# Performance work log

Measured on AMD Instinct MI355X. Metric: run time of the kernel, lower is better.

## Reference

```python
import jax, jax.numpy as jnp
import numpy as np

KSIZE = 8
STRIDE = 4
HEADS = 8
DIM_HEAD = 32
EPS = 1e-5


def _layernorm(x, g, b):
    m = jnp.mean(x, axis=-1, keepdims=True)
    v = jnp.mean(jnp.square(x - m), axis=-1, keepdims=True)
    return (x - m) / jnp.sqrt(v + EPS) * g + b


def setup_inputs() -> dict:
    key = jax.random.key(0)
    ks = jax.random.split(key, 4)
    B, H, W, C = 8, 64, 64, 256
    inner = HEADS * DIM_HEAD  # 256
    x = jax.random.normal(ks[0], (B, H, W, C), dtype=jnp.float32)
    return {
        "x": x,
        "ln1_g": jnp.ones((C,), jnp.float32),
        "ln1_b": jnp.zeros((C,), jnp.float32),
        "ln2_g": jnp.ones((C,), jnp.float32),
        "ln2_b": jnp.zeros((C,), jnp.float32),
        "w_qkv": jax.random.normal(ks[1], (C, inner * 3), jnp.float32) * 0.02,
        "w_out": jax.random.normal(ks[2], (inner, C), jnp.float32) * 0.02,
        "b_out": jnp.zeros((C,), jnp.float32),
    }


def reference(x, ln1_g, ln1_b, ln2_g, ln2_b, w_qkv, w_out, b_out):
    B, H, W, C = x.shape
    k, s = KSIZE, STRIDE
    nH = (H - k) // s + 1
    nW = (W - k) // s + 1
    L = nH * nW
    n = k * k  # tokens per window

    # window index grids (im2col / unfold)
    rows = jnp.arange(nH)[:, None] * s + jnp.arange(k)[None, :]  # [nH, k]
    cols = jnp.arange(nW)[:, None] * s + jnp.arange(k)[None, :]  # [nW, k]
    ridx = rows[:, None, :, None]  # [nH,1,k,1]
    cidx = cols[None, :, None, :]  # [1,nW,1,k]

    # unfold: [B, nH, nW, k, k, C] -> [(B L), (k k), C]
    patches = x[:, ridx, cidx, :].reshape(B * L, n, C)

    # LocalAttention2D.norm then AttentionBlock.norm
    p = _layernorm(patches, ln1_g, ln1_b)
    h = _layernorm(p, ln2_g, ln2_b)

    qkv = h @ w_qkv  # [(B L), n, 3*inner]
    q, kk, v = jnp.split(qkv, 3, axis=-1)
    q = q.reshape(B * L, n, HEADS, DIM_HEAD)
    kk = kk.reshape(B * L, n, HEADS, DIM_HEAD)
    v = v.reshape(B * L, n, HEADS, DIM_HEAD)

    scale = DIM_HEAD ** -0.5
    dots = jnp.einsum('bnhd,bmhd->bhnm', q, kk) * scale
    attn = jax.nn.softmax(dots, axis=-1)
    o = jnp.einsum('bhnm,bmhd->bnhd', attn, v).reshape(B * L, n, HEADS * DIM_HEAD)
    o = o @ w_out + b_out  # [(B L), n, C]

    # fold (col2im overlap-add)
    o = o.reshape(B, nH, nW, k, k, C)
    out = jnp.zeros((B, H, W, C), x.dtype).at[:, ridx, cidx, :].add(o)

    # normalization: fold(unfold(ones)) == overlap counts
    counts = jnp.zeros((H, W), x.dtype).at[ridx, cidx].add(1.0)
    return out / counts[None, :, :, None]
```

## Files before the change

kernel.cpp:

```cpp
#include <hip/hip_runtime.h>
#include <hip/hip_bf16.h>
#include <cstdint>
#include <cstddef>

#define LN_EPS 1e-5f
#define B_    8
#define HW_   64
#define C_    256
#define NTOK  (B_ * HW_ * HW_)
#define HEADS_ 8
#define DH_    32
#define NPATCH 15

__global__ __launch_bounds__(256) void ln_h_kernel(
    const float* __restrict__ x, const float* __restrict__ g1,
    const float* __restrict__ b1, const float* __restrict__ g2,
    const float* __restrict__ b2, float* __restrict__ h)
{
    const int gid  = blockIdx.x * 256 + threadIdx.x;
    const int tok  = gid >> 6;
    const int lane = gid & 63;
    if (tok >= NTOK) return;
    const float4 xv = reinterpret_cast<const float4*>(x + (size_t)tok * C_)[lane];
    float s  = xv.x + xv.y + xv.z + xv.w;
    float sq = xv.x*xv.x + xv.y*xv.y + xv.z*xv.z + xv.w*xv.w;
    for (int off = 32; off; off >>= 1) {
        s  += __shfl_xor(s, off);
        sq += __shfl_xor(sq, off);
    }
    const float m1 = s * (1.0f / 256.0f);
    const float r1 = rsqrtf(fmaxf(sq * (1.0f / 256.0f) - m1 * m1, 0.0f) + LN_EPS);
    const float4 g = reinterpret_cast<const float4*>(g1)[lane];
    const float4 b = reinterpret_cast<const float4*>(b1)[lane];
    const float y0 = (xv.x - m1) * r1 * g.x + b.x;
    const float y1 = (xv.y - m1) * r1 * g.y + b.y;
    const float y2 = (xv.z - m1) * r1 * g.z + b.z;
    const float y3 = (xv.w - m1) * r1 * g.w + b.w;
    float s2  = y0 + y1 + y2 + y3;
    float sq2 = y0*y0 + y1*y1 + y2*y2 + y3*y3;
    for (int off = 32; off; off >>= 1) {
        s2  += __shfl_xor(s2, off);
        sq2 += __shfl_xor(sq2, off);
    }
    const float m2 = s2 * (1.0f / 256.0f);
    const float r2 = rsqrtf(fmaxf(sq2 * (1.0f / 256.0f) - m2 * m2, 0.0f) + LN_EPS);
    const float4 G = reinterpret_cast<const float4*>(g2)[lane];
    const float4 B = reinterpret_cast<const float4*>(b2)[lane];
    float4 hv;
    hv.x = (y0 - m2) * r2 * G.x + B.x;
    hv.y = (y1 - m2) * r2 * G.y + B.y;
    hv.z = (y2 - m2) * r2 * G.z + B.z;
    hv.w = (y3 - m2) * r2 * G.w + B.w;
    reinterpret_cast<float4*>(h + (size_t)tok * C_)[lane] = hv;
}

__global__ __launch_bounds__(256) void qkv_h8_kernel(
    const float* __restrict__ h, const float* __restrict__ w, float* __restrict__ qkv)
{
    __shared__ float At[16][132];
    __shared__ float Bt[16][132];
    const int tid  = threadIdx.x;
    const int tok0 = blockIdx.y * 128;
    const int n0   = blockIdx.x * 128;
    const int ty = tid >> 4, tx = tid & 15;
    const int ar = tid >> 2, aseg = tid & 3;
    const int bk = tid >> 5, bn = tid & 31;
    const float* hrow0 = h + (size_t)(tok0 + ar) * C_;
    const float* hrow1 = h + (size_t)(tok0 + ar + 64) * C_;
    float acc[8][8] = {};
    for (int kk = 0; kk < 16; ++kk) {
        const int k0 = kk * 16;
        const float4 a0v = *reinterpret_cast<const float4*>(hrow0 + k0 + aseg * 4);
        const float4 a1v = *reinterpret_cast<const float4*>(hrow1 + k0 + aseg * 4);
        const float4 b0v = *reinterpret_cast<const float4*>(w + (size_t)(k0 + bk) * 768 + n0 + bn * 4);
        const float4 b1v = *reinterpret_cast<const float4*>(w + (size_t)(k0 + bk + 8) * 768 + n0 + bn * 4);
        __syncthreads();
        At[aseg*4+0][ar]    = a0v.x;
        At[aseg*4+1][ar]    = a0v.y;
        At[aseg*4+2][ar]    = a0v.z;
        At[aseg*4+3][ar]    = a0v.w;
        At[aseg*4+0][ar+64] = a1v.x;
        At[aseg*4+1][ar+64] = a1v.y;
        At[aseg*4+2][ar+64] = a1v.z;
        At[aseg*4+3][ar+64] = a1v.w;
        *reinterpret_cast<float4*>(&Bt[bk][bn*4])     = b0v;
        *reinterpret_cast<float4*>(&Bt[bk+8][bn*4])   = b1v;
        __syncthreads();
        #pragma unroll
        for (int k = 0; k < 16; ++k) {
            const float4 x0 = *reinterpret_cast<const float4*>(&At[k][ty*8]);
            const float4 x1 = *reinterpret_cast<const float4*>(&At[k][ty*8 + 4]);
            const float4 y0 = *reinterpret_cast<const float4*>(&Bt[k][tx*4]);
            const float4 y1 = *reinterpret_cast<const float4*>(&Bt[k][64 + tx*4]);
            const float a[8] = {x0.x, x0.y, x0.z, x0.w, x1.x, x1.y, x1.z, x1.w};
            const float b[8] = {y0.x, y0.y, y0.z, y0.w, y1.x, y1.y, y1.z, y1.w};
            #pragma unroll
            for (int i = 0; i < 8; ++i) {
                #pragma unroll
                for (int j = 0; j < 8; ++j)
                    acc[i][j] = fmaf(a[i], b[j], acc[i][j]);
            }
        }
    }
    #pragma unroll
    for (int i = 0; i < 8; ++i) {
        float* orow = qkv + (size_t)(tok0 + ty*8 + i) * 768 + n0;
        *reinterpret_cast<float4*>(orow + tx*4) =
            make_float4(acc[i][0], acc[i][1], acc[i][2], acc[i][3]);
        *reinterpret_cast<float4*>(orow + 64 + tx*4) =
            make_float4(acc[i][4], acc[i][5], acc[i][6], acc[i][7]);
    }
}

__global__ __launch_bounds__(256) void ln_stats_kernel(
    const float* __restrict__ x, const float* __restrict__ g1,
    const float* __restrict__ b1, float4* __restrict__ stats)
{
    const int gid  = blockIdx.x * 256 + threadIdx.x;
    const int tok  = gid >> 6;
    const int lane = gid & 63;
    if (tok >= NTOK) return;
    const float4 xv = reinterpret_cast<const float4*>(x + (size_t)tok * C_)[lane];
    float s  = xv.x + xv.y + xv.z + xv.w;
    float sq = xv.x*xv.x + xv.y*xv.y + xv.z*xv.z + xv.w*xv.w;
    for (int off = 32; off; off >>= 1) {
        s  += __shfl_xor(s, off);
        sq += __shfl_xor(sq, off);
    }
    const float m1 = s * (1.0f / 256.0f);
    const float r1 = rsqrtf(fmaxf(sq * (1.0f / 256.0f) - m1 * m1, 0.0f) + LN_EPS);
    const float4 g = reinterpret_cast<const float4*>(g1)[lane];
    const float4 b = reinterpret_cast<const float4*>(b1)[lane];
    const float y0 = (xv.x - m1) * r1 * g.x + b.x;
    const float y1 = (xv.y - m1) * r1 * g.y + b.y;
    const float y2 = (xv.z - m1) * r1 * g.z + b.z;
    const float y3 = (xv.w - m1) * r1 * g.w + b.w;
    float s2  = y0 + y1 + y2 + y3;
    float sq2 = y0*y0 + y1*y1 + y2*y2 + y3*y3;
    for (int off = 32; off; off >>= 1) {
        s2  += __shfl_xor(s2, off);
        sq2 += __shfl_xor(sq2, off);
    }
    const float m2 = s2 * (1.0f / 256.0f);
    const float r2 = rsqrtf(fmaxf(sq2 * (1.0f / 256.0f) - m2 * m2, 0.0f) + LN_EPS);
    if (lane == 0) stats[tok] = make_float4(m1, r1, m2, r2);
}

__global__ __launch_bounds__(256) void qkv_kernel(
    const float* __restrict__ x, const float4* __restrict__ stats,
    const float* __restrict__ g1, const float* __restrict__ b1,
    const float* __restrict__ g2, const float* __restrict__ b2,
    const float* __restrict__ w, float* __restrict__ qkv)
{
    __shared__ float At[16][72];
    __shared__ float Bt[16][64];
    const int tid  = threadIdx.x;
    const int tok0 = blockIdx.y * 64;
    const int n0   = blockIdx.x * 64;
    const int ty = tid >> 4, tx = tid & 15;
    const int st = tid >> 2, sseg = tid & 3;
    const int bk = tid >> 4, bx = tid & 15;
    const float4 s4 = stats[tok0 + st];
    const float* xrow = x + (size_t)(tok0 + st) * C_;
    float acc[4][4] = {};
    for (int kk = 0; kk < 16; ++kk) {
        const int k0 = kk * 16;
        const int ka = k0 + sseg * 4;
        const float4 xv  = *reinterpret_cast<const float4*>(xrow + ka);
        const float4 g1v = *reinterpret_cast<const float4*>(g1 + ka);
        const float4 b1v = *reinterpret_cast<const float4*>(b1 + ka);
        const float4 g2v = *reinterpret_cast<const float4*>(g2 + ka);
        const float4 b2v = *reinterpret_cast<const float4*>(b2 + ka);
        const float h0 = ((xv.x - s4.x)*s4.y*g1v.x + b1v.x - s4.z)*s4.w*g2v.x + b2v.x;
        const float h1 = ((xv.y - s4.x)*s4.y*g1v.y + b1v.y - s4.z)*s4.w*g2v.y + b2v.y;
        const float h2 = ((xv.z - s4.x)*s4.y*g1v.z + b1v.z - s4.z)*s4.w*g2v.z + b2v.z;
        const float h3 = ((xv.w - s4.x)*s4.y*g1v.w + b1v.w - s4.z)*s4.w*g2v.w + b2v.w;
        const float4 wv = *reinterpret_cast<const float4*>(w + (size_t)(k0 + bk) * 768 + n0 + bx * 4);
        __syncthreads();
        At[sseg*4+0][st] = h0;
        At[sseg*4+1][st] = h1;
        At[sseg*4+2][st] = h2;
        At[sseg*4+3][st] = h3;
        *reinterpret_cast<float4*>(&Bt[bk][bx*4]) = wv;
        __syncthreads();
        #pragma unroll
        for (int k = 0; k < 16; ++k) {
            const float4 a = *reinterpret_cast<const float4*>(&At[k][ty*4]);
            const float4 b = *reinterpret_cast<const float4*>(&Bt[k][tx*4]);
            acc[0][0] += a.x*b.x; acc[0][1] += a.x*b.y; acc[0][2] += a.x*b.z; acc[0][3] += a.x*b.w;
            acc[1][0] += a.y*b.x; acc[1][1] += a.y*b.y; acc[1][2] += a.y*b.z; acc[1][3] += a.y*b.w;
            acc[2][0] += a.z*b.x; acc[2][1] += a.z*b.y; acc[2][2] += a.z*b.z; acc[2][3] += a.z*b.w;
            acc[3][0] += a.w*b.x; acc[3][1] += a.w*b.y; acc[3][2] += a.w*b.z; acc[3][3] += a.w*b.w;
        }
    }
    #pragma unroll
    for (int r = 0; r < 4; ++r) {
        const float4 o = make_float4(acc[r][0], acc[r][1], acc[r][2], acc[r][3]);
        *reinterpret_cast<float4*>(qkv + (size_t)(tok0 + ty*4 + r) * 768 + n0 + tx*4) = o;
    }
}

__global__ __launch_bounds__(256) void attn_o_kernel(
    const float* __restrict__ qkv, float* __restrict__ obuf)
{
    __shared__ float smem[6784];
    float (*q_lds)[36] = reinterpret_cast<float(*)[36]>(smem);
    float (*kT)[68]    = reinterpret_cast<float(*)[68]>(smem + 2304);
    float (*v_lds)[36] = reinterpret_cast<float(*)[36]>(smem + 4480);
    float (*p_lds)[67] = reinterpret_cast<float(*)[67]>(smem);
    const int tid = threadIdx.x;
    const int b  = blockIdx.y;
    const int hd = blockIdx.z;
    const int pi = blockIdx.x / NPATCH;
    const int pj = blockIdx.x % NPATCH;
    const int t = tid >> 2, seg = tid & 3;
    const int pr = t >> 3, pc = t & 7;
    const size_t pixbase = ((size_t)((b * 64 + 4*pi + pr) * 64) + (4*pj + pc));
    {
        const size_t base = pixbase * 768 + hd * 32 + seg * 8;
        const float4 qa = *reinterpret_cast<const float4*>(qkv + base);
        const float4 qb = *reinterpret_cast<const float4*>(qkv + base + 4);
        const float4 ka = *reinterpret_cast<const float4*>(qkv + base + 256);
        const float4 kb = *reinterpret_cast<const float4*>(qkv + base + 260);
        const float4 va = *reinterpret_cast<const float4*>(qkv + base + 512);
        const float4 vb = *reinterpret_cast<const float4*>(qkv + base + 516);
        *reinterpret_cast<float4*>(&q_lds[t][seg*8    ]) = qa;
        *reinterpret_cast<float4*>(&q_lds[t][seg*8 + 4]) = qb;
        *reinterpret_cast<float4*>(&v_lds[t][seg*8    ]) = va;
        *reinterpret_cast<float4*>(&v_lds[t][seg*8 + 4]) = vb;
        const int d0 = seg * 8;
        kT[d0+0][t] = ka.x; kT[d0+1][t] = ka.y; kT[d0+2][t] = ka.z; kT[d0+3][t] = ka.w;
        kT[d0+4][t] = kb.x; kT[d0+5][t] = kb.y; kT[d0+6][t] = kb.z; kT[d0+7][t] = kb.w;
    }
    __syncthreads();
    const float scale = 0.17677669529663687f;
    const int tr = tid >> 4, tc = tid & 15;
    float s[4][4] = {};
    #pragma unroll
    for (int kk = 0; kk < 4; ++kk) {
        float qreg[4][8];
        #pragma unroll
        for (int i = 0; i < 4; ++i) {
            const float4 qv0 = *reinterpret_cast<const float4*>(&q_lds[tr*4 + i][kk*8]);
            const float4 qv1 = *reinterpret_cast<const float4*>(&q_lds[tr*4 + i][kk*8 + 4]);
            qreg[i][0] = qv0.x; qreg[i][1] = qv0.y; qreg[i][2] = qv0.z; qreg[i][3] = qv0.w;
            qreg[i][4] = qv1.x; qreg[i][5] = qv1.y; qreg[i][6] = qv1.z; qreg[i][7] = qv1.w;
        }
        #pragma unroll
        for (int w = 0; w < 8; ++w) {
            const float4 kv = *reinterpret_cast<const float4*>(&kT[kk*8 + w][tc*4]);
            const float ka[4] = {kv.x, kv.y, kv.z, kv.w};
            #pragma unroll
            for (int i = 0; i < 4; ++i) {
                #pragma unroll
                for (int j = 0; j < 4; ++j)
                    s[i][j] = fmaf(qreg[i][w], ka[j], s[i][j]);
            }
        }
    }
    float mrow[4], sum[4];
    #pragma unroll
    for (int i = 0; i < 4; ++i) {
        s[i][0] *= scale; s[i][1] *= scale; s[i][2] *= scale; s[i][3] *= scale;
        mrow[i] = fmaxf(fmaxf(s[i][0], s[i][1]), fmaxf(s[i][2], s[i][3]));
    }
    #pragma unroll
    for (int off = 1; off < 16; off <<= 1)
        #pragma unroll
        for (int i = 0; i < 4; ++i)
            mrow[i] = fmaxf(mrow[i], __shfl_xor(mrow[i], off));
    #pragma unroll
    for (int i = 0; i < 4; ++i) {
        sum[i] = 0.f;
        #pragma unroll
        for (int j = 0; j < 4; ++j) {
            s[i][j] = __expf(s[i][j] - mrow[i]);
            sum[i] += s[i][j];
        }
    }
    #pragma unroll
    for (int off = 1; off < 16; off <<= 1)
        #pragma unroll
        for (int i = 0; i < 4; ++i)
            sum[i] += __shfl_xor(sum[i], off);
    __syncthreads();
    #pragma unroll
    for (int i = 0; i < 4; ++i) {
        const float rs = 1.0f / sum[i];
        #pragma unroll
        for (int j = 0; j < 4; ++j)
            p_lds[tr*4 + i][tc*4 + j] = s[i][j] * rs;
    }
    __syncthreads();
    float4 o0 = make_float4(0,0,0,0), o1 = make_float4(0,0,0,0);
    for (int jc = 0; jc < 64; ++jc) {
        const float a = p_lds[t][jc];
        const float4 v0 = *reinterpret_cast<const float4*>(&v_lds[jc][seg*8]);
        const float4 v1 = *reinterpret_cast<const float4*>(&v_lds[jc][seg*8 + 4]);
        o0.x = fmaf(a, v0.x, o0.x); o0.y = fmaf(a, v0.y, o0.y);
        o0.z = fmaf(a, v0.z, o0.z); o0.w = fmaf(a, v0.w, o0.w);
        o1.x = fmaf(a, v1.x, o1.x); o1.y = fmaf(a, v1.y, o1.y);
        o1.z = fmaf(a, v1.z, o1.z); o1.w = fmaf(a, v1.w, o1.w);
    }
    float* op = obuf + ((size_t)(b * 225 + pi * NPATCH + pj) * 64 + t) * 256 + hd * 32 + seg * 8;
    *reinterpret_cast<float4*>(op)     = o0;
    *reinterpret_cast<float4*>(op + 4) = o1;
}

__global__ __launch_bounds__(256) void attn_kernel(
    const float* __restrict__ qkv, float* __restrict__ out,
    int gi, int gj, int nJ, int do_store)
{
    __shared__ float smem[6784];
    float (*q_lds)[36] = reinterpret_cast<float(*)[36]>(smem);
    float (*kT)[68]    = reinterpret_cast<float(*)[68]>(smem + 2304);
    float (*v_lds)[36] = reinterpret_cast<float(*)[36]>(smem + 4480);
    float (*p_lds)[67] = reinterpret_cast<float(*)[67]>(smem);
    const int tid = threadIdx.x;
    const int b  = blockIdx.y;
    const int hd = blockIdx.z;
    const int pi = 2 * (blockIdx.x / nJ) + gi;
    const int pj = 2 * (blockIdx.x % nJ) + gj;
    const int t = tid >> 2, seg = tid & 3;
    const int pr = t >> 3, pc = t & 7;
    const size_t pixbase = ((size_t)((b * 64 + 4*pi + pr) * 64) + (4*pj + pc));
    {
        const size_t base = pixbase * 768 + hd * 32 + seg * 8;
        const float4 qa = *reinterpret_cast<const float4*>(qkv + base);
        const float4 qb = *reinterpret_cast<const float4*>(qkv + base + 4);
        const float4 ka = *reinterpret_cast<const float4*>(qkv + base + 256);
        const float4 kb = *reinterpret_cast<const float4*>(qkv + base + 260);
        const float4 va = *reinterpret_cast<const float4*>(qkv + base + 512);
        const float4 vb = *reinterpret_cast<const float4*>(qkv + base + 516);
        *reinterpret_cast<float4*>(&q_lds[t][seg*8    ]) = qa;
        *reinterpret_cast<float4*>(&q_lds[t][seg*8 + 4]) = qb;
        *reinterpret_cast<float4*>(&v_lds[t][seg*8    ]) = va;
        *reinterpret_cast<float4*>(&v_lds[t][seg*8 + 4]) = vb;
        const int d0 = seg * 8;
        kT[d0+0][t] = ka.x; kT[d0+1][t] = ka.y; kT[d0+2][t] = ka.z; kT[d0+3][t] = ka.w;
        kT[d0+4][t] = kb.x; kT[d0+5][t] = kb.y; kT[d0+6][t] = kb.z; kT[d0+7][t] = kb.w;
    }
    __syncthreads();
    const float scale = 0.17677669529663687f;
    const int tr = tid >> 4, tc = tid & 15;
    float s[4][4] = {};
    #pragma unroll
    for (int kk = 0; kk < 4; ++kk) {
        float qreg[4][8];
        #pragma unroll
        for (int i = 0; i < 4; ++i) {
            const float4 qv0 = *reinterpret_cast<const float4*>(&q_lds[tr*4 + i][kk*8]);
            const float4 qv1 = *reinterpret_cast<const float4*>(&q_lds[tr*4 + i][kk*8 + 4]);
            qreg[i][0] = qv0.x; qreg[i][1] = qv0.y; qreg[i][2] = qv0.z; qreg[i][3] = qv0.w;
            qreg[i][4] = qv1.x; qreg[i][5] = qv1.y; qreg[i][6] = qv1.z; qreg[i][7] = qv1.w;
        }
        #pragma unroll
        for (int w = 0; w < 8; ++w) {
            const float4 kv = *reinterpret_cast<const float4*>(&kT[kk*8 + w][tc*4]);
            const float ka[4] = {kv.x, kv.y, kv.z, kv.w};
            #pragma unroll
            for (int i = 0; i < 4; ++i) {
                #pragma unroll
                for (int j = 0; j < 4; ++j)
                    s[i][j] = fmaf(qreg[i][w], ka[j], s[i][j]);
            }
        }
    }
    float mrow[4], sum[4];
    #pragma unroll
    for (int i = 0; i < 4; ++i) {
        s[i][0] *= scale; s[i][1] *= scale; s[i][2] *= scale; s[i][3] *= scale;
        mrow[i] = fmaxf(fmaxf(s[i][0], s[i][1]), fmaxf(s[i][2], s[i][3]));
    }
    #pragma unroll
    for (int off = 1; off < 16; off <<= 1)
        #pragma unroll
        for (int i = 0; i < 4; ++i)
            mrow[i] = fmaxf(mrow[i], __shfl_xor(mrow[i], off));
    #pragma unroll
    for (int i = 0; i < 4; ++i) {
        sum[i] = 0.f;
        #pragma unroll
        for (int j = 0; j < 4; ++j) {
            s[i][j] = __expf(s[i][j] - mrow[i]);
            sum[i] += s[i][j];
        }
    }
    #pragma unroll
    for (int off = 1; off < 16; off <<= 1)
        #pragma unroll
        for (int i = 0; i < 4; ++i)
            sum[i] += __shfl_xor(sum[i], off);
    __syncthreads();
    #pragma unroll
    for (int i = 0; i < 4; ++i) {
        const float rs = 1.0f / sum[i];
        #pragma unroll
        for (int j = 0; j < 4; ++j)
            p_lds[tr*4 + i][tc*4 + j] = s[i][j] * rs;
    }
    __syncthreads();
    float4 o0 = make_float4(0,0,0,0), o1 = make_float4(0,0,0,0);
    for (int jc = 0; jc < 64; ++jc) {
        const float a = p_lds[t][jc];
        const float4 v0 = *reinterpret_cast<const float4*>(&v_lds[jc][seg*8]);
        const float4 v1 = *reinterpret_cast<const float4*>(&v_lds[jc][seg*8 + 4]);
        o0.x = fmaf(a, v0.x, o0.x); o0.y = fmaf(a, v0.y, o0.y);
        o0.z = fmaf(a, v0.z, o0.z); o0.w = fmaf(a, v0.w, o0.w);
        o1.x = fmaf(a, v1.x, o1.x); o1.y = fmaf(a, v1.y, o1.y);
        o1.z = fmaf(a, v1.z, o1.z); o1.w = fmaf(a, v1.w, o1.w);
    }
    float* op = out + pixbase * 256 + hd * 32 + seg * 8;
    if (do_store) {
        *reinterpret_cast<float4*>(op)     = o0;
        *reinterpret_cast<float4*>(op + 4) = o1;
    } else {
        float4 c0 = *reinterpret_cast<const float4*>(op);
        float4 c1 = *reinterpret_cast<const float4*>(op + 4);
        c0.x += o0.x; c0.y += o0.y; c0.z += o0.z; c0.w += o0.w;
        c1.x += o1.x; c1.y += o1.y; c1.z += o1.z; c1.w += o1.w;
        *reinterpret_cast<float4*>(op)     = c0;
        *reinterpret_cast<float4*>(op + 4) = c1;
    }
}

__global__ __launch_bounds__(256) void proj_gather_kernel(
    const float* __restrict__ obuf, const float* __restrict__ w,
    const float* __restrict__ bo, float* __restrict__ out)
{
    __shared__ float At[16][36];
    __shared__ float Bt[16][256];
    const int tid  = threadIdx.x;
    const int tok0 = blockIdx.x * 32;
    const int ty = tid >> 5, tx = tid & 31;
    const int st = tid >> 2, sseg = tid & 3;
    const int bc = (tid & 63) * 4, bkb = tid >> 6;
    const float* s00 = obuf; const float* s01 = obuf;
    const float* s10 = obuf; const float* s11 = obuf;
    if (tid < 128) {
        const int token = tok0 + st;
        const int bb = token >> 12;
        const int hp = (token >> 6) & 63, wp = token & 63;
        const int pil = (hp >= 4) ? ((hp - 4) >> 2) : 0;
        const int pih = (hp >> 2) > 14 ? 14 : (hp >> 2);
        const int pjl = (wp >= 4) ? ((wp - 4) >> 2) : 0;
        const int pjh = (wp >> 2) > 14 ? 14 : (wp >> 2);
        const size_t base_b = (size_t)bb * 225;
        s00 = obuf + ((base_b + pil * NPATCH + pjl) * 64 + (8*(hp-4*pil) + (wp-4*pjl))) * 256;
        s01 = obuf + ((base_b + pil * NPATCH + pjh) * 64 + (8*(hp-4*pil) + (wp-4*pjh))) * 256;
        s10 = obuf + ((base_b + pih * NPATCH + pjl) * 64 + (8*(hp-4*pih) + (wp-4*pjl))) * 256;
        s11 = obuf + ((base_b + pih * NPATCH + pjh) * 64 + (8*(hp-4*pih) + (wp-4*pjh))) * 256;
    }
    float acc[4][8] = {};
    for (int kk = 0; kk < 16; ++kk) {
        const int k0 = kk * 16;
        float4 av = make_float4(0,0,0,0);
        if (tid < 128) {
            const int off = k0 + sseg * 4;
            const float4 v0 = *reinterpret_cast<const float4*>(s00 + off);
            const float4 v1 = *reinterpret_cast<const float4*>(s01 + off);
            const float4 v2 = *reinterpret_cast<const float4*>(s10 + off);
            const float4 v3 = *reinterpret_cast<const float4*>(s11 + off);
            av.x = ((v0.x + v1.x) + (v2.x + v3.x)) * 0.25f;
            av.y = ((v0.y + v1.y) + (v2.y + v3.y)) * 0.25f;
            av.z = ((v0.z + v1.z) + (v2.z + v3.z)) * 0.25f;
            av.w = ((v0.w + v1.w) + (v2.w + v3.w)) * 0.25f;
        }
        float4 wv[4];
        #pragma unroll
        for (int u = 0; u < 4; ++u)
            wv[u] = *reinterpret_cast<const float4*>(w + (size_t)(k0 + bkb*4 + u) * 256 + bc);
        __syncthreads();
        if (tid < 128) {
            At[sseg*4+0][st] = av.x;
            At[sseg*4+1][st] = av.y;
            At[sseg*4+2][st] = av.z;
            At[sseg*4+3][st] = av.w;
        }
        #pragma unroll
        for (int u = 0; u < 4; ++u)
            *reinterpret_cast<float4*>(&Bt[bkb*4+u][bc]) = wv[u];
        __syncthreads();
        #pragma unroll
        for (int k = 0; k < 16; ++k) {
            const float4 a  = *reinterpret_cast<const float4*>(&At[k][ty*4]);
            const float4 b0 = *reinterpret_cast<const float4*>(&Bt[k][tx*4]);
            const float4 b1 = *reinterpret_cast<const float4*>(&Bt[k][128 + tx*4]);
            acc[0][0] += a.x*b0.x; acc[0][1] += a.x*b0.y; acc[0][2] += a.x*b0.z; acc[0][3] += a.x*b0.w;
            acc[0][4] += a.x*b1.x; acc[0][5] += a.x*b1.y; acc[0][6] += a.x*b1.z; acc[0][7] += a.x*b1.w;
            acc[1][0] += a.y*b0.x; acc[1][1] += a.y*b0.y; acc[1][2] += a.y*b0.z; acc[1][3] += a.y*b0.w;
            acc[1][4] += a.y*b1.x; acc[1][5] += a.y*b1.y; acc[1][6] += a.y*b1.z; acc[1][7] += a.y*b1.w;
            acc[2][0] += a.z*b0.x; acc[2][1] += a.z*b0.y; acc[2][2] += a.z*b0.z; acc[2][3] += a.z*b0.w;
            acc[2][4] += a.z*b1.x; acc[2][5] += a.z*b1.y; acc[2][6] += a.z*b1.z; acc[2][7] += a.z*b1.w;
            acc[3][0] += a.w*b0.x; acc[3][1] += a.w*b0.y; acc[3][2] += a.w*b0.z; acc[3][3] += a.w*b0.w;
            acc[3][4] += a.w*b1.x; acc[3][5] += a.w*b1.y; acc[3][6] += a.w*b1.z; acc[3][7] += a.w*b1.w;
        }
    }
    const float4 bo0 = *reinterpret_cast<const float4*>(bo + tx*4);
    const float4 bo1 = *reinterpret_cast<const float4*>(bo + 128 + tx*4);
    #pragma unroll
    for (int r = 0; r < 4; ++r) {
        float* orow = out + (size_t)(tok0 + ty*4 + r) * 256;
        const float4 o0 = make_float4(acc[r][0]+bo0.x, acc[r][1]+bo0.y, acc[r][2]+bo0.z, acc[r][3]+bo0.w);
        const float4 o1 = make_float4(acc[r][4]+bo1.x, acc[r][5]+bo1.y, acc[r][6]+bo1.z, acc[r][7]+bo1.w);
        *reinterpret_cast<float4*>(orow + tx*4)       = o0;
        *reinterpret_cast<float4*>(orow + 128 + tx*4) = o1;
    }
}

__global__ __launch_bounds__(256) void proj_kernel(
    float* __restrict__ out, const float* __restrict__ w, const float* __restrict__ bo)
{
    __shared__ float At[16][36];
    __shared__ float Bt[16][256];
    const int tid  = threadIdx.x;
    const int tok0 = blockIdx.x * 32;
    const int ty = tid >> 5, tx = tid & 31;
    const int st = tid >> 2, sseg = tid & 3;
    const int bc = (tid & 63) * 4, bkb = tid >> 6;
    float ascale = 0.f;
    if (tid < 128) {
        const int token = tok0 + st;
        const int hp = (token >> 6) & 63, wp = token & 63;
        const float cnt = ((hp >= 4 && hp < 60) ? 2.f : 1.f) * ((wp >= 4 && wp < 60) ? 2.f : 1.f);
        ascale = 1.0f / cnt;
    }
    float acc[4][8] = {};
    for (int kk = 0; kk < 16; ++kk) {
        const int k0 = kk * 16;
        float4 av = make_float4(0,0,0,0);
        if (tid < 128)
            av = *reinterpret_cast<const float4*>(out + (size_t)(tok0 + st) * 256 + k0 + sseg * 4);
        float4 wv[4];
        #pragma unroll
        for (int u = 0; u < 4; ++u)
            wv[u] = *reinterpret_cast<const float4*>(w + (size_t)(k0 + bkb*4 + u) * 256 + bc);
        __syncthreads();
        if (tid < 128) {
            At[sseg*4+0][st] = av.x * ascale;
            At[sseg*4+1][st] = av.y * ascale;
            At[sseg*4+2][st] = av.z * ascale;
            At[sseg*4+3][st] = av.w * ascale;
        }
        #pragma unroll
        for (int u = 0; u < 4; ++u)
            *reinterpret_cast<float4*>(&Bt[bkb*4+u][bc]) = wv[u];
        __syncthreads();
        #pragma unroll
        for (int k = 0; k < 16; ++k) {
            const float4 a  = *reinterpret_cast<const float4*>(&At[k][ty*4]);
            const float4 b0 = *reinterpret_cast<const float4*>(&Bt[k][tx*4]);
            const float4 b1 = *reinterpret_cast<const float4*>(&Bt[k][128 + tx*4]);
            acc[0][0] += a.x*b0.x; acc[0][1] += a.x*b0.y; acc[0][2] += a.x*b0.z; acc[0][3] += a.x*b0.w;
            acc[0][4] += a.x*b1.x; acc[0][5] += a.x*b1.y; acc[0][6] += a.x*b1.z; acc[0][7] += a.x*b1.w;
            acc[1][0] += a.y*b0.x; acc[1][1] += a.y*b0.y; acc[1][2] += a.y*b0.z; acc[1][3] += a.y*b0.w;
            acc[1][4] += a.y*b1.x; acc[1][5] += a.y*b1.y; acc[1][6] += a.y*b1.z; acc[1][7] += a.y*b1.w;
            acc[2][0] += a.z*b0.x; acc[2][1] += a.z*b0.y; acc[2][2] += a.z*b0.z; acc[2][3] += a.z*b0.w;
            acc[2][4] += a.z*b1.x; acc[2][5] += a.z*b1.y; acc[2][6] += a.z*b1.z; acc[2][7] += a.z*b1.w;
            acc[3][0] += a.w*b0.x; acc[3][1] += a.w*b0.y; acc[3][2] += a.w*b0.z; acc[3][3] += a.w*b0.w;
            acc[3][4] += a.w*b1.x; acc[3][5] += a.w*b1.y; acc[3][6] += a.w*b1.z; acc[3][7] += a.w*b1.w;
        }
    }
    const float4 bo0 = *reinterpret_cast<const float4*>(bo + tx*4);
    const float4 bo1 = *reinterpret_cast<const float4*>(bo + 128 + tx*4);
    #pragma unroll
    for (int r = 0; r < 4; ++r) {
        float* orow = out + (size_t)(tok0 + ty*4 + r) * 256;
        const float4 o0 = make_float4(acc[r][0]+bo0.x, acc[r][1]+bo0.y, acc[r][2]+bo0.z, acc[r][3]+bo0.w);
        const float4 o1 = make_float4(acc[r][4]+bo1.x, acc[r][5]+bo1.y, acc[r][6]+bo1.z, acc[r][7]+bo1.w);
        *reinterpret_cast<float4*>(orow + tx*4)       = o0;
        *reinterpret_cast<float4*>(orow + 128 + tx*4) = o1;
    }
}

extern "C" void kernel_launch(void* const* d_in, const int* in_sizes, int n_in,
                              void* d_out, int out_size, void* d_ws, size_t ws_size,
                              hipStream_t stream)
{
    const float* x     = (const float*)d_in[0];
    const float* ln1_g = (const float*)d_in[1];
    const float* ln1_b = (const float*)d_in[2];
    const float* ln2_g = (const float*)d_in[3];
    const float* ln2_b = (const float*)d_in[4];
    const float* w_qkv = (const float*)d_in[5];
    const float* w_out = (const float*)d_in[6];
    const float* b_out = (const float*)d_in[7];
    float* out = (float*)d_out;
    char*  ws  = (char*)d_ws;

    const size_t h_b    = (size_t)NTOK * C_ * 4;
    const size_t qkv_b  = (size_t)NTOK * 768 * 4;
    const size_t obuf_b = (size_t)B_ * 225 * 64 * 256 * 4;
    const size_t stats_b = (size_t)NTOK * 16;

    if (ws_size >= h_b + qkv_b) {
        float* h    = (float*)ws;
        float* qkv  = (float*)(ws + h_b);
        float* obuf = (float*)(ws + h_b + qkv_b);
        ln_h_kernel<<<NTOK / 4, 256, 0, stream>>>(x, ln1_g, ln1_b, ln2_g, ln2_b, h);
        qkv_h8_kernel<<<dim3(6, NTOK / 128), 256, 0, stream>>>(h, w_qkv, qkv);
        if (ws_size >= h_b + qkv_b + obuf_b) {
            attn_o_kernel<<<dim3(225, B_, HEADS_), 256, 0, stream>>>(qkv, obuf);
            proj_gather_kernel<<<NTOK / 32, 256, 0, stream>>>(obuf, w_out, b_out, out);
        } else {
            for (int g = 0; g < 4; ++g) {
                const int gi = g >> 1, gj = g & 1;
                const int nI = gi ? 7 : 8, nJ = gj ? 7 : 8;
                attn_kernel<<<dim3(nI * nJ, B_, HEADS_), 256, 0, stream>>>(
                    qkv, out, gi, gj, nJ, (g == 0) ? 1 : 0);
            }
            proj_kernel<<<NTOK / 32, 256, 0, stream>>>(out, w_out, b_out);
        }
    } else {
        float4* stats = (float4*)ws;
        float*  qkv   = (float*)(ws + stats_b);
        ln_stats_kernel<<<NTOK / 4, 256, 0, stream>>>(x, ln1_g, ln1_b, stats);
        qkv_kernel<<<dim3(12, NTOK / 64), 256, 0, stream>>>(
            x, stats, ln1_g, ln1_b, ln2_g, ln2_b, w_qkv, qkv);
        for (int g = 0; g < 4; ++g) {
            const int gi = g >> 1, gj = g & 1;
            const int nI = gi ? 7 : 8, nJ = gj ? 7 : 8;
            attn_kernel<<<dim3(nI * nJ, B_, HEADS_), 256, 0, stream>>>(
                qkv, out, gi, gj, nJ, (g == 0) ? 1 : 0);
        }
        proj_kernel<<<NTOK / 32, 256, 0, stream>>>(out, w_out, b_out);
    }
}
```

Measured before the change: 430.7 us.

## Replace window attention with per-wavefront online-softmax kernel, four heads per block

Rewrites the windowed attention kernel so each 64-thread wavefront handles one head and each lane owns one query row. The row's scaled q stays in registers and the lane streams over keys with an online softmax that only rescales when the running max grows by more than 8. This removes the score tile in LDS, the shuffle reductions and two block barriers. Each block now covers four heads, so the grid shrinks by 4x, LDS per block grows, and the per-query work runs serially over 64 keys.

```diff
diff --git a/kernel.cpp b/kernel.cpp
--- a/kernel.cpp
+++ b/kernel.cpp
@@ -200,111 +200,88 @@
     }
 }
 
-__global__ __launch_bounds__(256) void attn_o_kernel(
+__global__ __launch_bounds__(256) void attn_flash_kernel(
     const float* __restrict__ qkv, float* __restrict__ obuf)
 {
-    __shared__ float smem[6784];
-    float (*q_lds)[36] = reinterpret_cast<float(*)[36]>(smem);
-    float (*kT)[68]    = reinterpret_cast<float(*)[68]>(smem + 2304);
-    float (*v_lds)[36] = reinterpret_cast<float(*)[36]>(smem + 4480);
-    float (*p_lds)[67] = reinterpret_cast<float(*)[67]>(smem);
-    const int tid = threadIdx.x;
-    const int b  = blockIdx.y;
-    const int hd = blockIdx.z;
-    const int pi = blockIdx.x / NPATCH;
-    const int pj = blockIdx.x % NPATCH;
-    const int t = tid >> 2, seg = tid & 3;
-    const int pr = t >> 3, pc = t & 7;
-    const size_t pixbase = ((size_t)((b * 64 + 4*pi + pr) * 64) + (4*pj + pc));
+    __shared__ float kbuf[4][64][33];
+    __shared__ float vbuf[4][64][33];
+    const int tid  = threadIdx.x;
+    const int wid  = tid >> 6;
+    const int lane = tid & 63;
+    const int b    = blockIdx.y;
+    const int hg   = blockIdx.z;
+    const int hd   = hg * 4 + wid;
+    const int pi   = blockIdx.x / NPATCH;
+    const int pj   = blockIdx.x % NPATCH;
+    const int rowbase = (b * 64 + 4*pi) * 64 + 4*pj;
+
     {
-        const size_t base = pixbase * 768 + hd * 32 + seg * 8;
-        const float4 qa = *reinterpret_cast<const float4*>(qkv + base);
-        const float4 qb = *reinterpret_cast<const float4*>(qkv + base + 4);
-        const float4 ka = *reinterpret_cast<const float4*>(qkv + base + 256);
-        const float4 kb = *reinterpret_cast<const float4*>(qkv + base + 260);
-        const float4 va = *reinterpret_cast<const float4*>(qkv + base + 512);
-        const float4 vb = *reinterpret_cast<const float4*>(qkv + base + 516);
-        *reinterpret_cast<float4*>(&q_lds[t][seg*8    ]) = qa;
-        *reinterpret_cast<float4*>(&q_lds[t][seg*8 + 4]) = qb;
-        *reinterpret_cast<float4*>(&v_lds[t][seg*8    ]) = va;
-        *reinterpret_cast<float4*>(&v_lds[t][seg*8 + 4]) = vb;
-        const int d0 = seg * 8;
-        kT[d0+0][t] = ka.x; kT[d0+1][t] = ka.y; kT[d0+2][t] = ka.z; kT[d0+3][t] = ka.w;
-        kT[d0+4][t] = kb.x; kT[d0+5][t] = kb.y; kT[d0+6][t] = kb.z; kT[d0+7][t] = kb.w;
+        const int pc = lane >> 3, f4 = lane & 7;
+        #pragma unroll
+        for (int i = 0; i < 8; ++i) {
+            const size_t pix = (size_t)rowbase + i * 64 + pc;
+            const float* src = qkv + pix * 768 + hd * 32 + f4 * 4;
+            const float4 kv4 = *reinterpret_cast<const float4*>(src + 256);
+            const float4 vv4 = *reinterpret_cast<const float4*>(src + 512);
+            *reinterpret_cast<float4*>(&kbuf[wid][i*8 + pc][f4*4]) = kv4;
+            *reinterpret_cast<float4*>(&vbuf[wid][i*8 + pc][f4*4]) = vv4;
+        }
+    }
+    const float scale = 0.17677669529663687f;
+    const int qpr = lane >> 3, qpc = lane & 7;
+    const float* qsrc = qkv + ((size_t)rowbase + qpr * 64 + qpc) * 768 + hd * 32;
+    float4 q4[8];
+    #pragma unroll
+    for (int u = 0; u < 8; ++u) {
+        float4 qv = *reinterpret_cast<const float4*>(qsrc + u * 4);
+        qv.x *= scale; qv.y *= scale; qv.z *= scale; qv.w *= scale;
+        q4[u] = qv;
     }
     __syncthreads();
-    const float scale = 0.17677669529663687f;
-    const int tr = tid >> 4, tc = tid & 15;
-    float s[4][4] = {};
-    #pragma unroll
-    for (int kk = 0; kk < 4; ++kk) {
-        float qreg[4][8];
-        #pragma unroll
-        for (int i = 0; i < 4; ++i) {
-            const float4 qv0 = *reinterpret_cast<const float4*>(&q_lds[tr*4 + i][kk*8]);
-            const float4 qv1 = *reinterpret_cast<const float4*>(&q_lds[tr*4 + i][kk*8 + 4]);
-            qreg[i][0] = qv0.x; qreg[i][1] = qv0.y; qreg[i][2] = qv0.z; qreg[i][3] = qv0.w;
-            qreg[i][4] = qv1.x; qreg[i][5] = qv1.y; qreg[i][6] = qv1.z; qreg[i][7] = qv1.w;
-        }
-        #pragma unroll
-        for (int w = 0; w < 8; ++w) {
-            const float4 kv = *reinterpret_cast<const float4*>(&kT[kk*8 + w][tc*4]);
-            const float ka[4] = {kv.x, kv.y, kv.z, kv.w};
+
+    float m = -1.0e30f, l = 0.0f;
+    float4 o4[8];
+    #pragma unroll
+    for (int u = 0; u < 8; ++u) o4[u] = make_float4(0.f, 0.f, 0.f, 0.f);
+
+    for (int jc = 0; jc < 64; ++jc) {
+        float a0 = 0.f, a1 = 0.f, a2 = 0.f, a3 = 0.f;
+        #pragma unroll
+        for (int u = 0; u < 8; ++u) {
+            const float4 kv = *reinterpret_cast<const float4*>(&kbuf[wid][jc][u*4]);
+            a0 = fmaf(q4[u].x, kv.x, a0);
+            a1 = fmaf(q4[u].y, kv.y, a1);
+            a2 = fmaf(q4[u].z, kv.z, a2);
+            a3 = fmaf(q4[u].w, kv.w, a3);
+        }
+        const float s = (a0 + a1) + (a2 + a3);
+        if (s > m + 8.0f) {
+            const float f = __expf(m - s);
+            m = s;
+            l *= f;
             #pragma unroll
-            for (int i = 0; i < 4; ++i) {
-                #pragma unroll
-                for (int j = 0; j < 4; ++j)
-                    s[i][j] = fmaf(qreg[i][w], ka[j], s[i][j]);
+            for (int u = 0; u < 8; ++u) {
+                o4[u].x *= f; o4[u].y *= f; o4[u].z *= f; o4[u].w *= f;
             }
         }
-    }
-    float mrow[4], sum[4];
-    #pragma unroll
-    for (int i = 0; i < 4; ++i) {
-        s[i][0] *= scale; s[i][1] *= scale; s[i][2] *= scale; s[i][3] *= scale;
-        mrow[i] = fmaxf(fmaxf(s[i][0], s[i][1]), fmaxf(s[i][2], s[i][3]));
-    }
-    #pragma unroll
-    for (int off = 1; off < 16; off <<= 1)
-        #pragma unroll
-        for (int i = 0; i < 4; ++i)
-            mrow[i] = fmaxf(mrow[i], __shfl_xor(mrow[i], off));
-    #pragma unroll
-    for (int i = 0; i < 4; ++i) {
-        sum[i] = 0.f;
-        #pragma unroll
-        for (int j = 0; j < 4; ++j) {
-            s[i][j] = __expf(s[i][j] - mrow[i]);
-            sum[i] += s[i][j];
-        }
-    }
-    #pragma unroll
-    for (int off = 1; off < 16; off <<= 1)
-        #pragma unroll
-        for (int i = 0; i < 4; ++i)
-            sum[i] += __shfl_xor(sum[i], off);
-    __syncthreads();
-    #pragma unroll
-    for (int i = 0; i < 4; ++i) {
-        const float rs = 1.0f / sum[i];
-        #pragma unroll
-        for (int j = 0; j < 4; ++j)
-            p_lds[tr*4 + i][tc*4 + j] = s[i][j] * rs;
-    }
-    __syncthreads();
-    float4 o0 = make_float4(0,0,0,0), o1 = make_float4(0,0,0,0);
-    for (int jc = 0; jc < 64; ++jc) {
-        const float a = p_lds[t][jc];
-        const float4 v0 = *reinterpret_cast<const float4*>(&v_lds[jc][seg*8]);
-        const float4 v1 = *reinterpret_cast<const float4*>(&v_lds[jc][seg*8 + 4]);
-        o0.x = fmaf(a, v0.x, o0.x); o0.y = fmaf(a, v0.y, o0.y);
-        o0.z = fmaf(a, v0.z, o0.z); o0.w = fmaf(a, v0.w, o0.w);
-        o1.x = fmaf(a, v1.x, o1.x); o1.y = fmaf(a, v1.y, o1.y);
-        o1.z = fmaf(a, v1.z, o1.z); o1.w = fmaf(a, v1.w, o1.w);
-    }
-    float* op = obuf + ((size_t)(b * 225 + pi * NPATCH + pj) * 64 + t) * 256 + hd * 32 + seg * 8;
-    *reinterpret_cast<float4*>(op)     = o0;
-    *reinterpret_cast<float4*>(op + 4) = o1;
+        const float p = __expf(s - m);
+        l += p;
+        #pragma unroll
+        for (int u = 0; u < 8; ++u) {
+            const float4 vv = *reinterpret_cast<const float4*>(&vbuf[wid][jc][u*4]);
+            o4[u].x = fmaf(p, vv.x, o4[u].x);
+            o4[u].y = fmaf(p, vv.y, o4[u].y);
+            o4[u].z = fmaf(p, vv.z, o4[u].z);
+            o4[u].w = fmaf(p, vv.w, o4[u].w);
+        }
+    }
+    const float rl = 1.0f / l;
+    float* op = obuf + ((size_t)(b * 225 + pi * NPATCH + pj) * 64 + lane) * 256 + hd * 32;
+    #pragma unroll
+    for (int u = 0; u < 8; ++u) {
+        *reinterpret_cast<float4*>(op + u * 4) =
+            make_float4(o4[u].x * rl, o4[u].y * rl, o4[u].z * rl, o4[u].w * rl);
+    }
 }
 
 __global__ __launch_bounds__(256) void attn_kernel(
@@ -600,7 +577,7 @@
         ln_h_kernel<<<NTOK / 4, 256, 0, stream>>>(x, ln1_g, ln1_b, ln2_g, ln2_b, h);
         qkv_h8_kernel<<<dim3(6, NTOK / 128), 256, 0, stream>>>(h, w_qkv, qkv);
         if (ws_size >= h_b + qkv_b + obuf_b) {
-            attn_o_kernel<<<dim3(225, B_, HEADS_), 256, 0, stream>>>(qkv, obuf);
+            attn_flash_kernel<<<dim3(225, B_, 2), 256, 0, stream>>>(qkv, obuf);
             proj_gather_kernel<<<NTOK / 32, 256, 0, stream>>>(obuf, w_out, b_out, out);
         } else {
             for (int g = 0; g < 4; ++g) {
```

New measurement: 566.1 us. 1.31x slower.

## Split overlap gather from output projection and use larger 128x128 GEMM tiles

Applied to the files above, without the earlier changes.

The fused gather+projection kernel is replaced by a separate gather kernel that averages the four overlapping window outputs into the reused h buffer, followed by a 128x128-tile projection GEMM with an 8x8 per-thread micro-tile. Previously each 32-token block re-read four obuf rows and used a small tile with half the threads idle during loads. The new layout raises arithmetic intensity and loads with all threads, at the cost of an extra write and read of an 8 MB-per-batch intermediate and one more launch.

```diff
diff --git a/kernel.cpp b/kernel.cpp
--- a/kernel.cpp
+++ b/kernel.cpp
@@ -424,87 +424,94 @@
     }
 }
 
-__global__ __launch_bounds__(256) void proj_gather_kernel(
-    const float* __restrict__ obuf, const float* __restrict__ w,
+__global__ __launch_bounds__(256) void gather_kernel(
+    const float* __restrict__ obuf, float* __restrict__ A)
+{
+    const int tid   = threadIdx.x;
+    const int token = blockIdx.x * 4 + (tid >> 6);
+    const int chunk = tid & 63;
+    const int bb = token >> 12;
+    const int hp = (token >> 6) & 63, wp = token & 63;
+    const int pil = (hp >= 4) ? ((hp - 4) >> 2) : 0;
+    const int pih = (hp >> 2) > 14 ? 14 : (hp >> 2);
+    const int pjl = (wp >= 4) ? ((wp - 4) >> 2) : 0;
+    const int pjh = (wp >> 2) > 14 ? 14 : (wp >> 2);
+    const size_t base_b = (size_t)bb * 225;
+    const float* s00 = obuf + ((base_b + pil * NPATCH + pjl) * 64 + (8*(hp-4*pil) + (wp-4*pjl))) * 256;
+    const float* s01 = obuf + ((base_b + pil * NPATCH + pjh) * 64 + (8*(hp-4*pil) + (wp-4*pjh))) * 256;
+    const float* s10 = obuf + ((base_b + pih * NPATCH + pjl) * 64 + (8*(hp-4*pih) + (wp-4*pjl))) * 256;
+    const float* s11 = obuf + ((base_b + pih * NPATCH + pjh) * 64 + (8*(hp-4*pih) + (wp-4*pjh))) * 256;
+    const int off = chunk * 4;
+    const float4 v0 = *reinterpret_cast<const float4*>(s00 + off);
+    const float4 v1 = *reinterpret_cast<const float4*>(s01 + off);
+    const float4 v2 = *reinterpret_cast<const float4*>(s10 + off);
+    const float4 v3 = *reinterpret_cast<const float4*>(s11 + off);
+    float4 a;
+    a.x = ((v0.x + v1.x) + (v2.x + v3.x)) * 0.25f;
+    a.y = ((v0.y + v1.y) + (v2.y + v3.y)) * 0.25f;
+    a.z = ((v0.z + v1.z) + (v2.z + v3.z)) * 0.25f;
+    a.w = ((v0.w + v1.w) + (v2.w + v3.w)) * 0.25f;
+    *reinterpret_cast<float4*>(A + (size_t)token * 256 + off) = a;
+}
+
+__global__ __launch_bounds__(256) void proj8_kernel(
+    const float* __restrict__ A, const float* __restrict__ w,
     const float* __restrict__ bo, float* __restrict__ out)
 {
-    __shared__ float At[16][36];
-    __shared__ float Bt[16][256];
+    __shared__ float At[16][132];
+    __shared__ float Bt[16][132];
     const int tid  = threadIdx.x;
-    const int tok0 = blockIdx.x * 32;
-    const int ty = tid >> 5, tx = tid & 31;
-    const int st = tid >> 2, sseg = tid & 3;
-    const int bc = (tid & 63) * 4, bkb = tid >> 6;
-    const float* s00 = obuf; const float* s01 = obuf;
-    const float* s10 = obuf; const float* s11 = obuf;
-    if (tid < 128) {
-        const int token = tok0 + st;
-        const int bb = token >> 12;
-        const int hp = (token >> 6) & 63, wp = token & 63;
-        const int pil = (hp >= 4) ? ((hp - 4) >> 2) : 0;
-        const int pih = (hp >> 2) > 14 ? 14 : (hp >> 2);
-        const int pjl = (wp >= 4) ? ((wp - 4) >> 2) : 0;
-        const int pjh = (wp >> 2) > 14 ? 14 : (wp >> 2);
-        const size_t base_b = (size_t)bb * 225;
-        s00 = obuf + ((base_b + pil * NPATCH + pjl) * 64 + (8*(hp-4*pil) + (wp-4*pjl))) * 256;
-        s01 = obuf + ((base_b + pil * NPATCH + pjh) * 64 + (8*(hp-4*pil) + (wp-4*pjh))) * 256;
-        s10 = obuf + ((base_b + pih * NPATCH + pjl) * 64 + (8*(hp-4*pih) + (wp-4*pjl))) * 256;
-        s11 = obuf + ((base_b + pih * NPATCH + pjh) * 64 + (8*(hp-4*pih) + (wp-4*pjh))) * 256;
-    }
-    float acc[4][8] = {};
+    const int tok0 = blockIdx.y * 128;
+    const int n0   = blockIdx.x * 128;
+    const int ty = tid >> 4, tx = tid & 15;
+    const int ar = tid >> 2, aseg = tid & 3;
+    const int bk = tid >> 5, bn = tid & 31;
+    const float* arow0 = A + (size_t)(tok0 + ar) * 256;
+    const float* arow1 = A + (size_t)(tok0 + ar + 64) * 256;
+    float acc[8][8] = {};
     for (int kk = 0; kk < 16; ++kk) {
         const int k0 = kk * 16;
-        float4 av = make_float4(0,0,0,0);
-        if (tid < 128) {
-            const int off = k0 + sseg * 4;
-            const float4 v0 = *reinterpret_cast<const float4*>(s00 + off);
-            const float4 v1 = *reinterpret_cast<const float4*>(s01 + off);
-            const float4 v2 = *reinterpret_cast<const float4*>(s10 + off);
-            const float4 v3 = *reinterpret_cast<const float4*>(s11 + off);
-            av.x = ((v0.x + v1.x) + (v2.x + v3.x)) * 0.25f;
-            av.y = ((v0.y + v1.y) + (v2.y + v3.y)) * 0.25f;
-            av.z = ((v0.z + v1.z) + (v2.z + v3.z)) * 0.25f;
-            av.w = ((v0.w + v1.w) + (v2.w + v3.w)) * 0.25f;
-        }
-        float4 wv[4];
-        #pragma unroll
-        for (int u = 0; u < 4; ++u)
-            wv[u] = *reinterpret_cast<const float4*>(w + (size_t)(k0 + bkb*4 + u) * 256 + bc);
-        __syncthreads();
-        if (tid < 128) {
-            At[sseg*4+0][st] = av.x;
-            At[sseg*4+1][st] = av.y;
-            At[sseg*4+2][st] = av.z;
-            At[sseg*4+3][st] = av.w;
-        }
-        #pragma unroll
-        for (int u = 0; u < 4; ++u)
-            *reinterpret_cast<float4*>(&Bt[bkb*4+u][bc]) = wv[u];
+        const float4 a0v = *reinterpret_cast<const float4*>(arow0 + k0 + aseg * 4);
+        const float4 a1v = *reinterpret_cast<const float4*>(arow1 + k0 + aseg * 4);
+        const float4 b0v = *reinterpret_cast<const float4*>(w + (size_t)(k0 + bk) * 256 + n0 + bn * 4);
+        const float4 b1v = *reinterpret_cast<const float4*>(w + (size_t)(k0 + bk + 8) * 256 + n0 + bn * 4);
+        __syncthreads();
+        At[aseg*4+0][ar]    = a0v.x;
+        At[aseg*4+1][ar]    = a0v.y;
+        At[aseg*4+2][ar]    = a0v.z;
+        At[aseg*4+3][ar]    = a0v.w;
+        At[aseg*4+0][ar+64] = a1v.x;
+        At[aseg*4+1][ar+64] = a1v.y;
+        At[aseg*4+2][ar+64] = a1v.z;
+        At[aseg*4+3][ar+64] = a1v.w;
+        *reinterpret_cast<float4*>(&Bt[bk][bn*4])   = b0v;
+        *reinterpret_cast<float4*>(&Bt[bk+8][bn*4]) = b1v;
         __syncthreads();
         #pragma unroll
         for (int k = 0; k < 16; ++k) {
-            const float4 a  = *reinterpret_cast<const float4*>(&At[k][ty*4]);
-            const float4 b0 = *reinterpret_cast<const float4*>(&Bt[k][tx*4]);
-            const float4 b1 = *reinterpret_cast<const float4*>(&Bt[k][128 + tx*4]);
-            acc[0][0] += a.x*b0.x; acc[0][1] += a.x*b0.y; acc[0][2] += a.x*b0.z; acc[0][3] += a.x*b0.w;
-            acc[0][4] += a.x*b1.x; acc[0][5] += a.x*b1.y; acc[0][6] += a.x*b1.z; acc[0][7] += a.x*b1.w;
-            acc[1][0] += a.y*b0.x; acc[1][1] += a.y*b0.y; acc[1][2] += a.y*b0.z; acc[1][3] += a.y*b0.w;
-            acc[1][4] += a.y*b1.x; acc[1][5] += a.y*b1.y; acc[1][6] += a.y*b1.z; acc[1][7] += a.y*b1.w;
-            acc[2][0] += a.z*b0.x; acc[2][1] += a.z*b0.y; acc[2][2] += a.z*b0.z; acc[2][3] += a.z*b0.w;
-            acc[2][4] += a.z*b1.x; acc[2][5] += a.z*b1.y; acc[2][6] += a.z*b1.z; acc[2][7] += a.z*b1.w;
-            acc[3][0] += a.w*b0.x; acc[3][1] += a.w*b0.y; acc[3][2] += a.w*b0.z; acc[3][3] += a.w*b0.w;
-            acc[3][4] += a.w*b1.x; acc[3][5] += a.w*b1.y; acc[3][6] += a.w*b1.z; acc[3][7] += a.w*b1.w;
-        }
-    }
-    const float4 bo0 = *reinterpret_cast<const float4*>(bo + tx*4);
-    const float4 bo1 = *reinterpret_cast<const float4*>(bo + 128 + tx*4);
-    #pragma unroll
-    for (int r = 0; r < 4; ++r) {
-        float* orow = out + (size_t)(tok0 + ty*4 + r) * 256;
-        const float4 o0 = make_float4(acc[r][0]+bo0.x, acc[r][1]+bo0.y, acc[r][2]+bo0.z, acc[r][3]+bo0.w);
-        const float4 o1 = make_float4(acc[r][4]+bo1.x, acc[r][5]+bo1.y, acc[r][6]+bo1.z, acc[r][7]+bo1.w);
-        *reinterpret_cast<float4*>(orow + tx*4)       = o0;
-        *reinterpret_cast<float4*>(orow + 128 + tx*4) = o1;
+            const float4 x0 = *reinterpret_cast<const float4*>(&At[k][ty*8]);
+            const float4 x1 = *reinterpret_cast<const float4*>(&At[k][ty*8 + 4]);
+            const float4 y0 = *reinterpret_cast<const float4*>(&Bt[k][tx*4]);
+            const float4 y1 = *reinterpret_cast<const float4*>(&Bt[k][64 + tx*4]);
+            const float a[8] = {x0.x, x0.y, x0.z, x0.w, x1.x, x1.y, x1.z, x1.w};
+            const float b[8] = {y0.x, y0.y, y0.z, y0.w, y1.x, y1.y, y1.z, y1.w};
+            #pragma unroll
+            for (int i = 0; i < 8; ++i) {
+                #pragma unroll
+                for (int j = 0; j < 8; ++j)
+                    acc[i][j] = fmaf(a[i], b[j], acc[i][j]);
+            }
+        }
+    }
+    const float4 bo0 = *reinterpret_cast<const float4*>(bo + n0 + tx*4);
+    const float4 bo1 = *reinterpret_cast<const float4*>(bo + n0 + 64 + tx*4);
+    #pragma unroll
+    for (int i = 0; i < 8; ++i) {
+        float* orow = out + (size_t)(tok0 + ty*8 + i) * 256 + n0;
+        *reinterpret_cast<float4*>(orow + tx*4) =
+            make_float4(acc[i][0]+bo0.x, acc[i][1]+bo0.y, acc[i][2]+bo0.z, acc[i][3]+bo0.w);
+        *reinterpret_cast<float4*>(orow + 64 + tx*4) =
+            make_float4(acc[i][4]+bo1.x, acc[i][5]+bo1.y, acc[i][6]+bo1.z, acc[i][7]+bo1.w);
     }
 }
 
@@ -601,7 +608,8 @@
         qkv_h8_kernel<<<dim3(6, NTOK / 128), 256, 0, stream>>>(h, w_qkv, qkv);
         if (ws_size >= h_b + qkv_b + obuf_b) {
             attn_o_kernel<<<dim3(225, B_, HEADS_), 256, 0, stream>>>(qkv, obuf);
-            proj_gather_kernel<<<NTOK / 32, 256, 0, stream>>>(obuf, w_out, b_out, out);
+            gather_kernel<<<NTOK / 4, 256, 0, stream>>>(obuf, h);
+            proj8_kernel<<<dim3(2, NTOK / 128), 256, 0, stream>>>(h, w_out, b_out, out);
         } else {
             for (int g = 0; g < 4; ++g) {
                 const int gi = g >> 1, gj = g & 1;
```

New measurement: 401.5 us, median of 2. 6.8% less time.
